# Kernel tuning notes

Hardware: AMD Instinct MI355X
Metric: run time of the kernel (lower is better)

Reference implementation:

```python
import jax, jax.numpy as jnp
import numpy as np

AMP = 3                 # half window
KS = 2 * AMP + 1        # kernel_size = 7
NUM_HEADS = 8


def setup_inputs() -> dict:
    key = jax.random.key(0)
    k1, k2 = jax.random.split(key)
    B, C, H, W = 8, 512, 96, 96
    x_q = jax.random.normal(k1, (B, C, H, W), dtype=jnp.float32)
    x_k = jax.random.normal(k2, (B, C, H, W), dtype=jnp.float32)
    return {"x_q": x_q, "x_k": x_k}


def _mov_forward(q, k):
    B, C, H, W = q.shape
    hd = C // NUM_HEADS
    scale = hd ** -0.5
    # (B, head_dim, n_heads, H, W) layout, exactly as the torch reshape
    qh = q.reshape(B, hd, NUM_HEADS, H, W) * scale
    kh = k.reshape(B, hd, NUM_HEADS, H, W)
    kp = jnp.pad(kh, ((0, 0), (0, 0), (0, 0), (AMP, AMP), (AMP, AMP)))

    hs = jnp.arange(H)
    ws = jnp.arange(W)
    attn = []
    for i in range(KS):
        vh = ((hs + i - AMP) >= 0) & ((hs + i - AMP) < H)  # valid rows for this offset
        for j in range(KS):
            vw = ((ws + j - AMP) >= 0) & ((ws + j - AMP) < W)
            # per-offset dot product over head_dim -> (B, nh, H, W)
            a = jnp.einsum('bdnhw,bdnhw->bnhw', qh, kp[:, :, :, i:i + H, j:j + W])
            valid = vh[:, None] & vw[None, :]  # (H, W)
            a = jnp.where(valid[None, None], a, jnp.float32(-1000.0))
            attn.append(a)
    attn = jnp.stack(attn, axis=1)            # (B, KS^2, nh, H, W)
    attn = jax.nn.softmax(attn, axis=1)       # softmax over the 49 offsets

    # relative-offset value vectors: grid of (di, dj) in [-AMP, AMP], row-major i,j
    offs = jnp.stack(
        jnp.meshgrid(jnp.arange(-AMP, AMP + 1), jnp.arange(-AMP, AMP + 1), indexing='ij'),
        axis=-1,
    ).reshape(KS * KS, 2).astype(attn.dtype)  # (KS^2, 2)

    v = jnp.einsum('bonhw,oc->bcnhw', attn, offs)  # (B, 2, nh, H, W)
    return jnp.mean(v, axis=2)                     # (B, 2, H, W)


def reference(x_q, x_k):
    return _mov_forward(x_q, x_k)
```

## Files before the change

### kernel.cpp

```cpp
#include <hip/hip_runtime.h>

#define BB 8
#define CC 512
#define NH 8
#define HD 64
#define HH 96
#define WW 96
#define AMP 3
#define KS 7
#define TH 16
#define TW 32
#define NTHR 256
#define HALO_H (TH + 2*AMP)
#define NGRP 10
#define LDSW 41
#define NPAIR 2
#define NCHUNK 16
#define PLANE (HH * WW)
#define NPLANE (NH * PLANE)
#define NTOT (BB * CC * PLANE)
#define TASKS (NPAIR * HALO_H * NGRP)
#define MAXS 2
#define LKHALF (NPAIR * HALO_H * LDSW)

typedef decltype(__builtin_amdgcn_cvt_pkrtz(0.f, 0.f)) h2;
typedef float f4 __attribute__((ext_vector_type(4)));

__device__ __forceinline__ void dot2a(float& c, h2 a, h2 b) {
    asm("v_dot2_f32_f16 %0, %1, %2, %0" : "+v"(c) : "v"(a), "v"(b));
}

__device__ __forceinline__ void barrier_nb() {
    asm volatile("s_waitcnt lgkmcnt(0)" ::: "memory");
    __builtin_amdgcn_s_barrier();
    asm volatile("" ::: "memory");
}

__global__ __launch_bounds__(NTHR, 2)
void mov_kernel(const float* __restrict__ q, const float* __restrict__ k,
                float* __restrict__ out) {
    const int tid = threadIdx.x;
    const int tx  = tid & 15;
    const int ty  = tid >> 4;
    const int bid  = blockIdx.x;
    const int n    = bid & 7;
    const int t2   = bid >> 3;
    const int b    = t2 / 18;
    const int tile = t2 - b * 18;
    const int th_i = tile / 3;
    const int tw_i = tile - th_i * 3;
    const int h0 = th_i * TH, w0 = tw_i * TW;
    const int h = h0 + ty, w = w0 + 2 * tx;

    __shared__ h2 lk[2 * LKHALF];

    int s_gpo[MAXS], s_lo[MAXS];
    bool s_v[MAXS];
#pragma unroll
    for (int s = 0; s < MAXS; ++s) {
        int id = tid + s * NTHR;
        s_v[s] = (id < TASKS);
        int id2 = s_v[s] ? id : 0;
        int p   = id2 / (HALO_H * NGRP);
        int rem = id2 - p * (HALO_H * NGRP);
        int r   = rem / NGRP;
        int g   = rem - r * NGRP;
        int y   = min(max(h0 + r - AMP, 0), HH - 1);
        s_gpo[s] = 2 * p * NPLANE + y * WW + (w0 - 4 + 4 * g);
        s_lo[s]  = (p * HALO_H + r) * LDSW + 4 * g;
    }

    const int kbase = (b * CC + n) * PLANE;
    const int qoff  = kbase + h * WW + w;
    const float scale = 0.125f;

    float acc0[KS * KS], acc1[KS * KS];
#pragma unroll
    for (int o = 0; o < KS * KS; ++o) { acc0[o] = 0.f; acc1[o] = 0.f; }

    f4 ska[MAXS], skb[MAXS];
    float2 qv[4];

    auto LOADK = [&](int c) {
#pragma unroll
        for (int s = 0; s < MAXS; ++s) {
            if (s_v[s]) {
                int base = kbase + c * 4 * NPLANE + s_gpo[s];
                int iA = min(max(base, 0), NTOT - 4);
                int iB = min(max(base + NPLANE, 0), NTOT - 4);
                ska[s] = *(const f4*)(k + iA);
                skb[s] = *(const f4*)(k + iB);
            }
        }
    };
    auto LOADQ = [&](int c) {
#pragma unroll
        for (int d = 0; d < 4; ++d)
            qv[d] = *(const float2*)(q + qoff + (c * 4 + d) * NPLANE);
    };
    auto WRITEK = [&](int buf) {
#pragma unroll
        for (int s = 0; s < MAXS; ++s) {
            if (s_v[s]) {
                h2* dst = &lk[buf * LKHALF + s_lo[s]];
#pragma unroll
                for (int u = 0; u < 4; ++u)
                    dst[u] = __builtin_amdgcn_cvt_pkrtz(ska[s][u], skb[s][u]);
            }
        }
    };

    LOADK(0);
    LOADQ(0);
    for (int c = 0; c < NCHUNK; ++c) {
        const int buf = c & 1;
        WRITEK(buf);
        if (c + 1 < NCHUNK) LOADK(c + 1);
        h2 qq0[NPAIR], qq1[NPAIR];
#pragma unroll
        for (int p = 0; p < NPAIR; ++p) {
            qq0[p] = __builtin_amdgcn_cvt_pkrtz(qv[2 * p].x * scale, qv[2 * p + 1].x * scale);
            qq1[p] = __builtin_amdgcn_cvt_pkrtz(qv[2 * p].y * scale, qv[2 * p + 1].y * scale);
        }
        if (c + 1 < NCHUNK) LOADQ(c + 1);
        barrier_nb();
#pragma unroll
        for (int p = 0; p < NPAIR; ++p) {
#pragma unroll
            for (int i = 0; i < KS; ++i) {
                const int rb = buf * LKHALF + (p * HALO_H + ty + i) * LDSW + 2 * tx + 1;
                h2 kv[8];
#pragma unroll
                for (int t = 0; t < 8; ++t) kv[t] = lk[rb + t];
#pragma unroll
                for (int j = 0; j < KS; ++j) {
                    dot2a(acc0[i * KS + j], qq0[p], kv[j]);
                    dot2a(acc1[i * KS + j], qq1[p], kv[j + 1]);
                }
            }
        }
        barrier_nb();
    }

#pragma unroll
    for (int i = 0; i < KS; ++i) {
        bool vi = ((unsigned)(h + i - AMP) < HH);
#pragma unroll
        for (int j = 0; j < KS; ++j) {
            bool v0 = vi && ((unsigned)(w + j - AMP) < WW);
            bool v1 = vi && ((unsigned)(w + 1 + j - AMP) < WW);
            if (!v0) acc0[i * KS + j] = -1e30f;
            if (!v1) acc1[i * KS + j] = -1e30f;
        }
    }

    float m0 = -1e30f, m1 = -1e30f;
#pragma unroll
    for (int o = 0; o < KS * KS; ++o) {
        m0 = fmaxf(m0, acc0[o]);
        m1 = fmaxf(m1, acc1[o]);
    }
    float l0 = 0.f, di0 = 0.f, dj0 = 0.f;
    float l1 = 0.f, di1 = 0.f, dj1 = 0.f;
#pragma unroll
    for (int i = 0; i < KS; ++i) {
#pragma unroll
        for (int j = 0; j < KS; ++j) {
            float e0 = __expf(acc0[i * KS + j] - m0);
            float e1 = __expf(acc1[i * KS + j] - m1);
            l0 += e0; l1 += e1;
            di0 += e0 * (float)(i - AMP);
            di1 += e1 * (float)(i - AMP);
            dj0 += e0 * (float)(j - AMP);
            dj1 += e1 * (float)(j - AMP);
        }
    }
    float inv0 = 1.0f / (l0 * (float)NH);
    float inv1 = 1.0f / (l1 * (float)NH);

    float* o0 = out + ((size_t)b * 2 + 0) * PLANE + h * WW + w;
    float* o1 = out + ((size_t)b * 2 + 1) * PLANE + h * WW + w;
    atomicAdd(o0,     di0 * inv0);
    atomicAdd(o0 + 1, di1 * inv1);
    atomicAdd(o1,     dj0 * inv0);
    atomicAdd(o1 + 1, dj1 * inv1);
}

extern "C" void kernel_launch(void* const* d_in, const int* in_sizes, int n_in,
                              void* d_out, int out_size, void* d_ws, size_t ws_size,
                              hipStream_t stream) {
    const float* q = (const float*)d_in[0];
    const float* k = (const float*)d_in[1];
    float* out = (float*)d_out;

    hipMemsetAsync(out, 0, (size_t)out_size * sizeof(float), stream);

    dim3 grid(BB * NH * (HH / TH) * (WW / TW));
    dim3 block(NTHR);
    hipLaunchKernelGGL(mov_kernel, grid, block, 0, stream, q, k, out);
}
```

Measured before the change: 92.60 us.

## Interleave four channels per LDS column with 128-bit accesses and drop the trailing barrier

The K tile in LDS is re-laid out so each column holds all four channels of a chunk as two packed half2 values. This lets both staging writes and compute reads use 128-bit LDS operations instead of many 32-bit ones, and each staging thread now loads four channel planes in one task. The second barrier per chunk is removed because the double-buffer ordering already separates reads from the next overwrite. The min-blocks launch bound is also dropped, which may change register allocation and occupancy.

```diff
diff --git a/kernel.cpp b/kernel.cpp
--- a/kernel.cpp
+++ b/kernel.cpp
@@ -12,19 +12,20 @@
 #define TW 32
 #define NTHR 256
 #define HALO_H (TH + 2*AMP)
-#define NGRP 10
-#define LDSW 41
-#define NPAIR 2
+#define NCOL 40
+#define ROWH2 (NCOL * 2)
+#define LKSZ (HALO_H * ROWH2)
 #define NCHUNK 16
 #define PLANE (HH * WW)
 #define NPLANE (NH * PLANE)
 #define NTOT (BB * CC * PLANE)
-#define TASKS (NPAIR * HALO_H * NGRP)
-#define MAXS 2
-#define LKHALF (NPAIR * HALO_H * LDSW)
+#define TASKS (HALO_H * 10)
 
 typedef decltype(__builtin_amdgcn_cvt_pkrtz(0.f, 0.f)) h2;
 typedef float f4 __attribute__((ext_vector_type(4)));
+typedef _Float16 h8 __attribute__((ext_vector_type(8)));
+
+union H8U { h8 v; h2 h[4]; };
 
 __device__ __forceinline__ void dot2a(float& c, h2 a, h2 b) {
     asm("v_dot2_f32_f16 %0, %1, %2, %0" : "+v"(c) : "v"(a), "v"(b));
@@ -36,7 +37,7 @@
     asm volatile("" ::: "memory");
 }
 
-__global__ __launch_bounds__(NTHR, 2)
+__global__ __launch_bounds__(NTHR)
 void mov_kernel(const float* __restrict__ q, const float* __restrict__ k,
                 float* __restrict__ out) {
     const int tid = threadIdx.x;
@@ -52,23 +53,14 @@
     const int h0 = th_i * TH, w0 = tw_i * TW;
     const int h = h0 + ty, w = w0 + 2 * tx;
 
-    __shared__ h2 lk[2 * LKHALF];
-
-    int s_gpo[MAXS], s_lo[MAXS];
-    bool s_v[MAXS];
-#pragma unroll
-    for (int s = 0; s < MAXS; ++s) {
-        int id = tid + s * NTHR;
-        s_v[s] = (id < TASKS);
-        int id2 = s_v[s] ? id : 0;
-        int p   = id2 / (HALO_H * NGRP);
-        int rem = id2 - p * (HALO_H * NGRP);
-        int r   = rem / NGRP;
-        int g   = rem - r * NGRP;
-        int y   = min(max(h0 + r - AMP, 0), HH - 1);
-        s_gpo[s] = 2 * p * NPLANE + y * WW + (w0 - 4 + 4 * g);
-        s_lo[s]  = (p * HALO_H + r) * LDSW + 4 * g;
-    }
+    __shared__ h2 lk[2 * LKSZ];
+
+    const bool sv = (tid < TASKS);
+    const int r_  = sv ? tid / 10 : 0;
+    const int g_  = sv ? tid - r_ * 10 : 0;
+    const int y_  = min(max(h0 + r_ - AMP, 0), HH - 1);
+    const int sgo = y_ * WW + (w0 - 4 + 4 * g_);
+    const int slo = r_ * ROWH2 + 8 * g_;
 
     const int kbase = (b * CC + n) * PLANE;
     const int qoff  = kbase + h * WW + w;
@@ -78,19 +70,20 @@
 #pragma unroll
     for (int o = 0; o < KS * KS; ++o) { acc0[o] = 0.f; acc1[o] = 0.f; }
 
-    f4 ska[MAXS], skb[MAXS];
+    f4 ka, kb, kc, kd;
     float2 qv[4];
 
     auto LOADK = [&](int c) {
-#pragma unroll
-        for (int s = 0; s < MAXS; ++s) {
-            if (s_v[s]) {
-                int base = kbase + c * 4 * NPLANE + s_gpo[s];
-                int iA = min(max(base, 0), NTOT - 4);
-                int iB = min(max(base + NPLANE, 0), NTOT - 4);
-                ska[s] = *(const f4*)(k + iA);
-                skb[s] = *(const f4*)(k + iB);
-            }
+        if (sv) {
+            int base = kbase + c * 4 * NPLANE + sgo;
+            int i0 = min(max(base,              0), NTOT - 4);
+            int i1 = min(max(base +     NPLANE, 0), NTOT - 4);
+            int i2 = min(max(base + 2 * NPLANE, 0), NTOT - 4);
+            int i3 = min(max(base + 3 * NPLANE, 0), NTOT - 4);
+            ka = *(const f4*)(k + i0);
+            kb = *(const f4*)(k + i1);
+            kc = *(const f4*)(k + i2);
+            kd = *(const f4*)(k + i3);
         }
     };
     auto LOADQ = [&](int c) {
@@ -99,14 +92,19 @@
             qv[d] = *(const float2*)(q + qoff + (c * 4 + d) * NPLANE);
     };
     auto WRITEK = [&](int buf) {
-#pragma unroll
-        for (int s = 0; s < MAXS; ++s) {
-            if (s_v[s]) {
-                h2* dst = &lk[buf * LKHALF + s_lo[s]];
-#pragma unroll
-                for (int u = 0; u < 4; ++u)
-                    dst[u] = __builtin_amdgcn_cvt_pkrtz(ska[s][u], skb[s][u]);
-            }
+        if (sv) {
+            H8U u0, u1;
+            u0.h[0] = __builtin_amdgcn_cvt_pkrtz(ka.x, kb.x);
+            u0.h[1] = __builtin_amdgcn_cvt_pkrtz(kc.x, kd.x);
+            u0.h[2] = __builtin_amdgcn_cvt_pkrtz(ka.y, kb.y);
+            u0.h[3] = __builtin_amdgcn_cvt_pkrtz(kc.y, kd.y);
+            u1.h[0] = __builtin_amdgcn_cvt_pkrtz(ka.z, kb.z);
+            u1.h[1] = __builtin_amdgcn_cvt_pkrtz(kc.z, kd.z);
+            u1.h[2] = __builtin_amdgcn_cvt_pkrtz(ka.w, kb.w);
+            u1.h[3] = __builtin_amdgcn_cvt_pkrtz(kc.w, kd.w);
+            h2* dst = &lk[buf * LKSZ + slo];
+            *(h8*)(dst)     = u0.v;
+            *(h8*)(dst + 4) = u1.v;
         }
     };
 
@@ -116,30 +114,32 @@
         const int buf = c & 1;
         WRITEK(buf);
         if (c + 1 < NCHUNK) LOADK(c + 1);
-        h2 qq0[NPAIR], qq1[NPAIR];
-#pragma unroll
-        for (int p = 0; p < NPAIR; ++p) {
-            qq0[p] = __builtin_amdgcn_cvt_pkrtz(qv[2 * p].x * scale, qv[2 * p + 1].x * scale);
-            qq1[p] = __builtin_amdgcn_cvt_pkrtz(qv[2 * p].y * scale, qv[2 * p + 1].y * scale);
-        }
+        h2 qA0 = __builtin_amdgcn_cvt_pkrtz(qv[0].x * scale, qv[1].x * scale);
+        h2 qB0 = __builtin_amdgcn_cvt_pkrtz(qv[2].x * scale, qv[3].x * scale);
+        h2 qA1 = __builtin_amdgcn_cvt_pkrtz(qv[0].y * scale, qv[1].y * scale);
+        h2 qB1 = __builtin_amdgcn_cvt_pkrtz(qv[2].y * scale, qv[3].y * scale);
         if (c + 1 < NCHUNK) LOADQ(c + 1);
         barrier_nb();
 #pragma unroll
-        for (int p = 0; p < NPAIR; ++p) {
-#pragma unroll
-            for (int i = 0; i < KS; ++i) {
-                const int rb = buf * LKHALF + (p * HALO_H + ty + i) * LDSW + 2 * tx + 1;
-                h2 kv[8];
-#pragma unroll
-                for (int t = 0; t < 8; ++t) kv[t] = lk[rb + t];
-#pragma unroll
-                for (int j = 0; j < KS; ++j) {
-                    dot2a(acc0[i * KS + j], qq0[p], kv[j]);
-                    dot2a(acc1[i * KS + j], qq1[p], kv[j + 1]);
-                }
+        for (int i = 0; i < KS; ++i) {
+            const h2* row = &lk[buf * LKSZ + (ty + i) * ROWH2 + 4 * tx];
+            h2 kvA[10], kvB[10];
+#pragma unroll
+            for (int m = 0; m < 5; ++m) {
+                H8U u; u.v = *(const h8*)(row + 4 * m);
+                kvA[2 * m]     = u.h[0];
+                kvB[2 * m]     = u.h[1];
+                kvA[2 * m + 1] = u.h[2];
+                kvB[2 * m + 1] = u.h[3];
             }
-        }
-        barrier_nb();
+#pragma unroll
+            for (int j = 0; j < KS; ++j) {
+                dot2a(acc0[i * KS + j], qA0, kvA[j + 1]);
+                dot2a(acc0[i * KS + j], qB0, kvB[j + 1]);
+                dot2a(acc1[i * KS + j], qA1, kvA[j + 2]);
+                dot2a(acc1[i * KS + j], qB1, kvB[j + 2]);
+            }
+        }
     }
 
 #pragma unroll
```

Result: faster. 85.88 us (-7.3%).
